# Optimization experiments

Hardware: AMD Instinct MI355X
Metric: run time of the kernel (lower is better)

## Reference

```python
import jax, jax.numpy as jnp
import numpy as np

B, S, D, H = 2, 2048, 1024, 16
DK = D // H


def setup_inputs() -> dict:
    key = jax.random.key(0)
    ks = jax.random.split(key, 11)
    scale = 1.0 / np.sqrt(D)
    inp = {
        "k": jax.random.normal(ks[0], (B, S, D), jnp.float32),
        "q": jax.random.normal(ks[1], (B, S, D), jnp.float32),
        "v": jax.random.normal(ks[2], (B, S, D), jnp.float32),
        "w_q": jax.random.normal(ks[3], (D, D), jnp.float32) * scale,
        "b_q": jax.random.normal(ks[4], (D,), jnp.float32) * 0.01,
        "w_k": jax.random.normal(ks[5], (D, D), jnp.float32) * scale,
        "b_k": jax.random.normal(ks[6], (D,), jnp.float32) * 0.01,
        "w_v": jax.random.normal(ks[7], (D, D), jnp.float32) * scale,
        "b_v": jax.random.normal(ks[8], (D,), jnp.float32) * 0.01,
        "w_o": jax.random.normal(ks[9], (D, D), jnp.float32) * scale,
        "b_o": jax.random.normal(ks[10], (D,), jnp.float32) * 0.01,
        # causal mask; positions with mask==0 get -1e9 (masked_fill semantics)
        "mask": jnp.tril(jnp.ones((1, 1, S, S), jnp.int32)),
    }
    return inp


def reference(k, q, v, w_q, b_q, w_k, b_k, w_v, b_v, w_o, b_o, mask):
    MINUS_INF = -1000000000.0

    def proj(x, w, b):
        # nn.Linear: x @ w.T + b, then split heads -> [B, H, S, DK]
        y = x @ w.T + b
        return y.reshape(B, S, H, DK).transpose(0, 2, 1, 3)

    Q = proj(q, w_q, b_q)
    K = proj(k, w_k, b_k)
    V = proj(v, w_v, b_v)

    # [B, H, Sq, Sk] scores
    scores = jnp.einsum("bhqd,bhkd->bhqk", Q, K) / jnp.sqrt(jnp.float32(DK))
    scores = jnp.where(mask == 0, MINUS_INF, scores)
    attn = jax.nn.softmax(scores, axis=-1)

    out = jnp.einsum("bhqk,bhkd->bhqd", attn, V)  # [B, H, S, DK]
    out = out.transpose(0, 2, 1, 3).reshape(B, S, D)  # concat heads
    return out @ w_o.T + b_o
```

## Files before the change

kernel.cpp:

```cpp
#include <hip/hip_runtime.h>

typedef __bf16 bf16;
typedef __bf16 v8bf __attribute__((ext_vector_type(8)));
typedef __bf16 v4bf __attribute__((ext_vector_type(4)));
typedef float  v4f  __attribute__((ext_vector_type(4)));

#define MFMA16(a,b,c) __builtin_amdgcn_mfma_f32_16x16x32_bf16((a),(b),(c),0,0,0)

static constexpr int Sq = 2048;
static constexpr size_t NI = 4194304;
static constexpr size_t NW = 1048576;

__device__ __forceinline__ void gld_lds16(const void* g, void* l) {
  __builtin_amdgcn_global_load_lds(
      (__attribute__((address_space(1))) unsigned int*)g,
      (__attribute__((address_space(3))) unsigned int*)l,
      16, 0, 0);
}

__device__ __forceinline__ float exp2_raw(float x) {
  return __builtin_amdgcn_exp2f(x);
}

__global__ __launch_bounds__(256) void convert_kernel(
    const float* __restrict__ q, const float* __restrict__ k, const float* __restrict__ v,
    const float* __restrict__ wq, const float* __restrict__ wk,
    const float* __restrict__ wv, const float* __restrict__ wo,
    bf16* __restrict__ dst)
{
  const int NI4 = 1048576;
  const int NW4 = 262144;
  int idx = blockIdx.x * 256 + threadIdx.x;
  const float* src; size_t dstoff; int local;
  if (idx < 3 * NI4) {
    int a = idx >> 20; local = idx & (NI4 - 1);
    src = (a == 0) ? q : ((a == 1) ? k : v);
    dstoff = (size_t)a * NI;
  } else {
    int t = idx - 3 * NI4;
    int a = t >> 18; local = t & (NW4 - 1);
    src = (a == 0) ? wq : ((a == 1) ? wk : ((a == 2) ? wv : wo));
    dstoff = 3 * NI + (size_t)a * NW;
  }
  float4 f = ((const float4*)src)[local];
  v4bf hv = { (bf16)f.x, (bf16)f.y, (bf16)f.z, (bf16)f.w };
  *(v4bf*)(dst + dstoff + (size_t)local * 4) = hv;
}

__device__ __forceinline__ void gemm_bt_body(
    const bf16* __restrict__ A, const bf16* __restrict__ Bw,
    const float* __restrict__ bias, bf16* __restrict__ outh,
    int bm, int bn, int mode)
{
  __shared__ alignas(16) bf16 As[128 * 32];
  __shared__ alignas(16) bf16 Bs[128 * 32];
  const int tid = threadIdx.x;
  const int wave = tid >> 6, lane = tid & 63;
  const int quad = lane >> 4, l15 = lane & 15;
  const int wm = (wave >> 1) * 64, wn = (wave & 1) * 64;
  const int lrow = lane >> 2, lcol = (lane & 3) * 8;

  v4f acc[4][4];
#pragma unroll
  for (int i = 0; i < 4; i++)
#pragma unroll
    for (int j = 0; j < 4; j++) { v4f z = {0.f, 0.f, 0.f, 0.f}; acc[i][j] = z; }

  const bf16* gA = A  + (size_t)(bm + wave * 32 + lrow) * 1024 + lcol;
  const bf16* gB = Bw + (size_t)(bn + wave * 32 + lrow) * 1024 + lcol;
  bf16* lA0 = &As[(wave * 32) * 32];
  bf16* lA1 = &As[(wave * 32 + 16) * 32];
  bf16* lB0 = &Bs[(wave * 32) * 32];
  bf16* lB1 = &Bs[(wave * 32 + 16) * 32];

  for (int k0 = 0; k0 < 1024; k0 += 32) {
    gld_lds16(gA + k0, lA0);
    gld_lds16(gA + 16 * 1024 + k0, lA1);
    gld_lds16(gB + k0, lB0);
    gld_lds16(gB + 16 * 1024 + k0, lB1);
    __syncthreads();
    v8bf af[4], bfr[4];
#pragma unroll
    for (int i = 0; i < 4; i++)
      af[i] = *(const v8bf*)&As[(wm + i * 16 + l15) * 32 + quad * 8];
#pragma unroll
    for (int j = 0; j < 4; j++)
      bfr[j] = *(const v8bf*)&Bs[(wn + j * 16 + l15) * 32 + quad * 8];
#pragma unroll
    for (int i = 0; i < 4; i++)
#pragma unroll
      for (int j = 0; j < 4; j++)
        acc[i][j] = MFMA16(af[i], bfr[j], acc[i][j]);
    __syncthreads();
  }

#pragma unroll
  for (int i = 0; i < 4; i++) {
    const int m0 = bm + wm + i * 16 + quad * 4;
#pragma unroll
    for (int j = 0; j < 4; j++) {
      const int n = bn + wn + j * 16 + l15;
      const float bv = bias[n];
      if (mode == 2) {
        int b_ = m0 >> 11, s_ = m0 & 2047;
        int h_ = n >> 6,  dk = n & 63;
        v4bf pk;
#pragma unroll
        for (int r = 0; r < 4; r++) pk[r] = (bf16)(acc[i][j][r] + bv);
        *(v4bf*)&outh[((size_t)((b_ * 16 + h_) * 64 + dk)) * 2048 + s_] = pk;
      } else {
        const float sc = (mode == 3) ? 0.18033688011112042f : 1.0f;
        int h_ = n >> 6,  dk = n & 63;
#pragma unroll
        for (int r = 0; r < 4; r++) {
          int m = m0 + r;
          int b_ = m >> 11, s_ = m & 2047;
          outh[(((size_t)(b_ * 16 + h_) * 2048 + s_) << 6) + dk] =
              (bf16)((acc[i][j][r] + bv) * sc);
        }
      }
    }
  }
}

__global__ __launch_bounds__(256, 2) void gemm_proj_kernel(
    const bf16* qb, const bf16* kb, const bf16* vb,
    const bf16* wqb, const bf16* wkb, const bf16* wvb,
    const float* bq, const float* bk, const float* bv,
    bf16* Qh, bf16* Kh, bf16* VhT)
{
  const bf16* A; const bf16* W; const float* bias; bf16* out; int mode;
  if (blockIdx.z == 0)      { A = qb; W = wqb; bias = bq; out = Qh;  mode = 3; }
  else if (blockIdx.z == 1) { A = kb; W = wkb; bias = bk; out = Kh;  mode = 0; }
  else                      { A = vb; W = wvb; bias = bv; out = VhT; mode = 2; }
  gemm_bt_body(A, W, bias, out, blockIdx.y * 128, blockIdx.x * 128, mode);
}

__global__ __launch_bounds__(256, 4) void gemm_final_kernel(
    const bf16* __restrict__ Ob, const bf16* __restrict__ wob,
    const float* __restrict__ bo, float* __restrict__ out)
{
  __shared__ alignas(16) bf16 As[64 * 32];
  __shared__ alignas(16) bf16 Bs[128 * 32];
  const int bm = blockIdx.y * 64, bn = blockIdx.x * 128;
  const int tid = threadIdx.x;
  const int wave = tid >> 6, lane = tid & 63;
  const int quad = lane >> 4, l15 = lane & 15;
  const int wm = (wave >> 1) * 32, wn = (wave & 1) * 64;
  const int lrow = lane >> 2, lcol = (lane & 3) * 8;

  v4f acc[2][4];
#pragma unroll
  for (int i = 0; i < 2; i++)
#pragma unroll
    for (int j = 0; j < 4; j++) { v4f z = {0.f, 0.f, 0.f, 0.f}; acc[i][j] = z; }

  const bf16* gA = Ob  + (size_t)(bm + wave * 16 + lrow) * 1024 + lcol;
  const bf16* gB = wob + (size_t)(bn + wave * 32 + lrow) * 1024 + lcol;
  bf16* lA  = &As[(wave * 16) * 32];
  bf16* lB0 = &Bs[(wave * 32) * 32];
  bf16* lB1 = &Bs[(wave * 32 + 16) * 32];

  for (int k0 = 0; k0 < 1024; k0 += 32) {
    gld_lds16(gA + k0, lA);
    gld_lds16(gB + k0, lB0);
    gld_lds16(gB + 16 * 1024 + k0, lB1);
    __syncthreads();
    v8bf af[2], bfr[4];
#pragma unroll
    for (int i = 0; i < 2; i++)
      af[i] = *(const v8bf*)&As[(wm + i * 16 + l15) * 32 + quad * 8];
#pragma unroll
    for (int j = 0; j < 4; j++)
      bfr[j] = *(const v8bf*)&Bs[(wn + j * 16 + l15) * 32 + quad * 8];
#pragma unroll
    for (int i = 0; i < 2; i++)
#pragma unroll
      for (int j = 0; j < 4; j++)
        acc[i][j] = MFMA16(af[i], bfr[j], acc[i][j]);
    __syncthreads();
  }

#pragma unroll
  for (int i = 0; i < 2; i++) {
    const int m0 = bm + wm + i * 16 + quad * 4;
#pragma unroll
    for (int j = 0; j < 4; j++) {
      const int n = bn + wn + j * 16 + l15;
      const float bv = bo[n];
#pragma unroll
      for (int r = 0; r < 4; r++)
        out[(size_t)(m0 + r) * 1024 + n] = acc[i][j][r] + bv;
    }
  }
}

__global__ __launch_bounds__(128, 2) void attn_kernel(
    const bf16* __restrict__ Qh, const bf16* __restrict__ Kh,
    const bf16* __restrict__ VhT, bf16* __restrict__ Ob)
{
  __shared__ alignas(16) bf16 Ps[2][32 * 72];
  const int tid = threadIdx.x;
  const int wave = tid >> 6, lane = tid & 63;
  const int quad = lane >> 4, l15 = lane & 15;
  const int bh = blockIdx.x, gy = blockIdx.y;
  const int b = bh >> 4, h = bh & 15;
  const int r8 = gy & 7, q8 = gy >> 3;
  const int u = 8 * q8 + ((q8 & 1) ? (7 - r8) : r8);
  const int qt = 2 * u + wave;
  const int L = u;
  const bf16* Qb = Qh + (size_t)bh * Sq * 64;
  const bf16* Kb = Kh + (size_t)bh * Sq * 64;
  const bf16* Vb = VhT + (size_t)bh * 64 * Sq;
  bf16* Pw = &Ps[wave][0];
  const int r0 = qt * 32;

  v8bf aq[2][2];
#pragma unroll
  for (int s = 0; s < 2; s++)
#pragma unroll
    for (int ks = 0; ks < 2; ks++)
      aq[s][ks] = *(const v8bf*)&Qb[(size_t)(r0 + s * 16 + l15) * 64 + ks * 32 + quad * 8];

  float lsum[2][4];
  v4f o[2][4];
#pragma unroll
  for (int s = 0; s < 2; s++)
#pragma unroll
    for (int r = 0; r < 4; r++) lsum[s][r] = 0.f;
#pragma unroll
  for (int s = 0; s < 2; s++)
#pragma unroll
    for (int j = 0; j < 4; j++) { v4f z = {0.f, 0.f, 0.f, 0.f}; o[s][j] = z; }

  auto loadK = [&](int kb, v8bf (&BK)[4][2]) {
#pragma unroll
    for (int n = 0; n < 4; n++) {
      BK[n][0] = *(const v8bf*)&Kb[(size_t)(kb + n * 16 + l15) * 64 + quad * 8];
      BK[n][1] = *(const v8bf*)&Kb[(size_t)(kb + n * 16 + l15) * 64 + 32 + quad * 8];
    }
  };
  auto loadV = [&](int kb, v8bf (&BV)[4][2]) {
#pragma unroll
    for (int n = 0; n < 4; n++) {
      BV[n][0] = *(const v8bf*)&Vb[(size_t)(n * 16 + l15) * 2048 + kb + quad * 8];
      BV[n][1] = *(const v8bf*)&Vb[(size_t)(n * 16 + l15) * 2048 + kb + 32 + quad * 8];
    }
  };
  auto compute = [&](const v8bf (&BK)[4][2], const v8bf (&BV)[4][2], int kc, bool diag) {
    const int kbase = kc * 64;
#pragma unroll
    for (int s = 0; s < 2; s++) {
      v4f cn[4];
#pragma unroll
      for (int n = 0; n < 4; n++) {
        v4f z = {0.f, 0.f, 0.f, 0.f};
        cn[n] = MFMA16(aq[s][0], BK[n][0], z);
        cn[n] = MFMA16(aq[s][1], BK[n][1], cn[n]);
      }
      const int rbase = r0 + s * 16 + quad * 4;
#pragma unroll
      for (int n = 0; n < 4; n++) {
        const int colg = kbase + n * 16 + l15;
#pragma unroll
        for (int r = 0; r < 4; r++) {
          float e = exp2_raw(cn[n][r]);
          if (diag && colg > rbase + r) e = 0.f;
          lsum[s][r] += e;
          Pw[(s * 16 + quad * 4 + r) * 72 + n * 16 + l15] = (bf16)e;
        }
      }
    }
#pragma unroll
    for (int s = 0; s < 2; s++) {
      v8bf ap0 = *(const v8bf*)&Pw[(s * 16 + l15) * 72 + quad * 8];
      v8bf ap1 = *(const v8bf*)&Pw[(s * 16 + l15) * 72 + 32 + quad * 8];
#pragma unroll
      for (int j = 0; j < 4; j++) {
        o[s][j] = MFMA16(ap0, BV[j][0], o[s][j]);
        o[s][j] = MFMA16(ap1, BV[j][1], o[s][j]);
      }
    }
  };

  v8bf bk0[4][2], bk1[4][2], bvv[4][2];
  loadK(0, bk0);
  int kc = 0;
  while (kc < L) {
    loadV(kc * 64, bvv);
    loadK((kc + 1) * 64, bk1);
    compute(bk0, bvv, kc, false);
    ++kc;
    if (kc >= L) {
      loadV(kc * 64, bvv);
      compute(bk1, bvv, kc, true);
      kc = -1;
      break;
    }
    loadV(kc * 64, bvv);
    loadK((kc + 1) * 64, bk0);
    compute(bk1, bvv, kc, false);
    ++kc;
  }
  if (kc >= 0) {
    loadV(kc * 64, bvv);
    compute(bk0, bvv, kc, true);
  }

#pragma unroll
  for (int s = 0; s < 2; s++)
#pragma unroll
    for (int r = 0; r < 4; r++) {
#pragma unroll
      for (int off = 1; off < 16; off <<= 1)
        lsum[s][r] += __shfl_xor(lsum[s][r], off, 64);
    }
#pragma unroll
  for (int s = 0; s < 2; s++)
#pragma unroll
    for (int r = 0; r < 4; r++) {
      const float inv = 1.0f / lsum[s][r];
      const int sg = r0 + s * 16 + quad * 4 + r;
#pragma unroll
      for (int j = 0; j < 4; j++)
        Ob[((size_t)(b * Sq + sg)) * 1024 + h * 64 + j * 16 + l15] =
            (bf16)(o[s][j][r] * inv);
    }
}

extern "C" void kernel_launch(void* const* d_in, const int* in_sizes, int n_in,
                              void* d_out, int out_size, void* d_ws, size_t ws_size,
                              hipStream_t stream) {
  (void)in_sizes; (void)n_in; (void)out_size; (void)ws_size;
  const float* kin = (const float*)d_in[0];
  const float* qin = (const float*)d_in[1];
  const float* vin = (const float*)d_in[2];
  const float* wq  = (const float*)d_in[3];
  const float* bq  = (const float*)d_in[4];
  const float* wk  = (const float*)d_in[5];
  const float* bk  = (const float*)d_in[6];
  const float* wv  = (const float*)d_in[7];
  const float* bv  = (const float*)d_in[8];
  const float* wo  = (const float*)d_in[9];
  const float* bo  = (const float*)d_in[10];

  bf16* ws = (bf16*)d_ws;
  bf16* qb  = ws;
  bf16* kb  = ws + NI;
  bf16* vb  = ws + 2 * NI;
  bf16* wqb = ws + 3 * NI;
  bf16* wkb = wqb + NW;
  bf16* wvb = wqb + 2 * NW;
  bf16* wob = wqb + 3 * NW;
  bf16* Qh  = ws + 3 * NI + 4 * NW;
  bf16* Kh  = Qh + NI;
  bf16* VhT = Qh + 2 * NI;
  bf16* Ob  = Qh + 3 * NI;

  convert_kernel<<<16384, 256, 0, stream>>>(qin, kin, vin, wq, wk, wv, wo, ws);
  gemm_proj_kernel<<<dim3(8, 32, 3), 256, 0, stream>>>(
      qb, kb, vb, wqb, wkb, wvb, bq, bk, bv, Qh, Kh, VhT);
  attn_kernel<<<dim3(32, 32), 128, 0, stream>>>(Qh, Kh, VhT, Ob);
  gemm_final_kernel<<<dim3(8, 64), 256, 0, stream>>>(Ob, wob, bo, (float*)d_out);
}
```

Baseline: 254.3 us.

## Split long causal query tiles across two waves and merge partial sums in LDS

Before, each block held two waves, each handling an adjacent 32-row query tile over the causal key range. Now the grid grows to 48 slots per head. The 16 longest pairs of tiles are broken into single tiles, each split along the key axis between the two waves. The partial outputs and row sums are combined through shared memory, and short tiles keep the old two-waves-per-block layout. The goal is to even out per-wave work under the causal triangle and cut tail imbalance, at the cost of more blocks, extra LDS use and a block-wide barrier. The split appears to rely on the softmax having no running max, so partial sums can simply be added.

```diff
diff --git a/kernel.cpp b/kernel.cpp
--- a/kernel.cpp
+++ b/kernel.cpp
@@ -200,14 +200,29 @@
     const bf16* __restrict__ VhT, bf16* __restrict__ Ob)
 {
   __shared__ alignas(16) bf16 Ps[2][32 * 72];
+  __shared__ alignas(16) float Osum[32][66];
+  __shared__ float Lsum[32];
   const int tid = threadIdx.x;
   const int wave = tid >> 6, lane = tid & 63;
   const int quad = lane >> 4, l15 = lane & 15;
-  const int bh = blockIdx.x, gy = blockIdx.y;
+  const int bh = blockIdx.x, slot = blockIdx.y;
   const int b = bh >> 4, h = bh & 15;
-  const int r8 = gy & 7, q8 = gy >> 3;
-  const int u = 8 * q8 + ((q8 & 1) ? (7 - r8) : r8);
-  const int qt = 2 * u + wave;
+
+  const int g = slot >> 3, c = slot & 7;
+  int u, qt, lo, hi; bool split;
+  if (g == 2 || g == 5) {
+    u = (g == 2) ? 15 - c : c;
+    qt = 2 * u + wave;
+    lo = 0; hi = u; split = false;
+  } else {
+    u = (g < 2) ? 31 - c : 16 + c;
+    const int parity = (g == 1 || g == 4) ? 1 : 0;
+    qt = 2 * u + parity;
+    const int m = (u + 2) >> 1;
+    lo = wave ? m : 0;
+    hi = wave ? u : (m - 1);
+    split = true;
+  }
   const int L = u;
   const bf16* Qb = Qh + (size_t)bh * Sq * 64;
   const bf16* Kb = Kh + (size_t)bh * Sq * 64;
@@ -283,28 +298,30 @@
     }
   };
 
-  v8bf bk0[4][2], bk1[4][2], bvv[4][2];
-  loadK(0, bk0);
-  int kc = 0;
-  while (kc < L) {
-    loadV(kc * 64, bvv);
-    loadK((kc + 1) * 64, bk1);
-    compute(bk0, bvv, kc, false);
-    ++kc;
-    if (kc >= L) {
+  {
+    v8bf bk0[4][2], bk1[4][2], bvv[4][2];
+    loadK(lo * 64, bk0);
+    int kc = lo;
+    while (kc < hi) {
       loadV(kc * 64, bvv);
-      compute(bk1, bvv, kc, true);
-      kc = -1;
-      break;
-    }
-    loadV(kc * 64, bvv);
-    loadK((kc + 1) * 64, bk0);
-    compute(bk1, bvv, kc, false);
-    ++kc;
-  }
-  if (kc >= 0) {
-    loadV(kc * 64, bvv);
-    compute(bk0, bvv, kc, true);
+      loadK((kc + 1) * 64, bk1);
+      compute(bk0, bvv, kc, false);
+      ++kc;
+      if (kc >= hi) {
+        loadV(kc * 64, bvv);
+        compute(bk1, bvv, kc, kc == L);
+        kc = -1;
+        break;
+      }
+      loadV(kc * 64, bvv);
+      loadK((kc + 1) * 64, bk0);
+      compute(bk1, bvv, kc, false);
+      ++kc;
+    }
+    if (kc >= 0) {
+      loadV(kc * 64, bvv);
+      compute(bk0, bvv, kc, kc == L);
+    }
   }
 
 #pragma unroll
@@ -315,17 +332,51 @@
       for (int off = 1; off < 16; off <<= 1)
         lsum[s][r] += __shfl_xor(lsum[s][r], off, 64);
     }
-#pragma unroll
-  for (int s = 0; s < 2; s++)
-#pragma unroll
-    for (int r = 0; r < 4; r++) {
-      const float inv = 1.0f / lsum[s][r];
-      const int sg = r0 + s * 16 + quad * 4 + r;
+
+  if (split && wave == 1) {
+#pragma unroll
+    for (int s = 0; s < 2; s++)
 #pragma unroll
       for (int j = 0; j < 4; j++)
-        Ob[((size_t)(b * Sq + sg)) * 1024 + h * 64 + j * 16 + l15] =
-            (bf16)(o[s][j][r] * inv);
-    }
+#pragma unroll
+        for (int r = 0; r < 4; r++)
+          Osum[s * 16 + quad * 4 + r][j * 16 + l15] = o[s][j][r];
+    if (l15 == 0) {
+#pragma unroll
+      for (int s = 0; s < 2; s++)
+#pragma unroll
+        for (int r = 0; r < 4; r++)
+          Lsum[s * 16 + quad * 4 + r] = lsum[s][r];
+    }
+  }
+  __syncthreads();
+
+  if (!split) {
+#pragma unroll
+    for (int s = 0; s < 2; s++)
+#pragma unroll
+      for (int r = 0; r < 4; r++) {
+        const float inv = 1.0f / lsum[s][r];
+        const int sg = r0 + s * 16 + quad * 4 + r;
+#pragma unroll
+        for (int j = 0; j < 4; j++)
+          Ob[((size_t)(b * Sq + sg)) * 1024 + h * 64 + j * 16 + l15] =
+              (bf16)(o[s][j][r] * inv);
+      }
+  } else if (wave == 0) {
+#pragma unroll
+    for (int s = 0; s < 2; s++)
+#pragma unroll
+      for (int r = 0; r < 4; r++) {
+        const int row = s * 16 + quad * 4 + r;
+        const float inv = 1.0f / (lsum[s][r] + Lsum[row]);
+        const int sg = r0 + row;
+#pragma unroll
+        for (int j = 0; j < 4; j++)
+          Ob[((size_t)(b * Sq + sg)) * 1024 + h * 64 + j * 16 + l15] =
+              (bf16)((o[s][j][r] + Osum[row][j * 16 + l15]) * inv);
+      }
+  }
 }
 
 extern "C" void kernel_launch(void* const* d_in, const int* in_sizes, int n_in,
@@ -360,6 +411,6 @@
   convert_kernel<<<16384, 256, 0, stream>>>(qin, kin, vin, wq, wk, wv, wo, ws);
   gemm_proj_kernel<<<dim3(8, 32, 3), 256, 0, stream>>>(
       qb, kb, vb, wqb, wkb, wvb, bq, bk, bv, Qh, Kh, VhT);
-  attn_kernel<<<dim3(32, 32), 128, 0, stream>>>(Qh, Kh, VhT, Ob);
+  attn_kernel<<<dim3(32, 48), 128, 0, stream>>>(Qh, Kh, VhT, Ob);
   gemm_final_kernel<<<dim3(8, 64), 256, 0, stream>>>(Ob, wob, bo, (float*)d_out);
 }
```

New measurement: 266.6 us. 1.05x slower.
